# Kernel tuning notes

Hardware: AMD Instinct MI355X
Metric: run time of the kernel (lower is better)

Reference implementation:

```python
import jax, jax.numpy as jnp
import numpy as np

B, T, D = 4, 2048, 1024
H = 16
HD = D // H  # 64


def setup_inputs() -> dict:
    key = jax.random.key(0)
    k1, k2, k3 = jax.random.split(key, 3)
    x = jax.random.normal(k1, (B, T, D), dtype=jnp.float32)
    w_qkv = jax.random.normal(k2, (D, 3 * D), dtype=jnp.float32) * (1.0 / np.sqrt(D))
    w_out = jax.random.normal(k3, (D, D), dtype=jnp.float32) * (1.0 / np.sqrt(D))
    return {"x": x, "w_qkv": w_qkv, "w_out": w_out}


def reference(x, w_qkv, w_out):
    b, t, c = x.shape
    qkv = x @ w_qkv  # [B,T,3D]
    q, k, v = jnp.split(qkv, 3, axis=-1)

    def heads(u):
        return u.reshape(b, t, H, HD).transpose(0, 2, 1, 3)  # [B,H,T,HD]

    q, k, v = heads(q), heads(k), heads(v)
    scale = 1.0 / np.sqrt(HD).astype(np.float32)
    attn = jnp.einsum('bhqd,bhkd->bhqk', q, k) * scale  # [B,H,T,T]
    causal = jnp.tril(jnp.ones((t, t), dtype=bool))
    attn = jnp.where(causal[None, None, :, :], attn, -jnp.inf)
    attn = jax.nn.softmax(attn, axis=-1)
    y = jnp.einsum('bhqk,bhkd->bhqd', attn, v)  # [B,H,T,HD]
    y = y.transpose(0, 2, 1, 3).reshape(b, t, c)
    return y @ w_out
```

## Files before the change

kernel.cpp:

```cpp
#include <hip/hip_runtime.h>
#include <hip/hip_bf16.h>
#include <stdint.h>

#define B_    4
#define T_    2048
#define D_    1024
#define H_    16
#define HD_   64
#define ROWS_ (B_ * T_)
#define NQKV_ (3 * D_)

typedef __attribute__((ext_vector_type(8))) short bf16x8;
typedef __attribute__((ext_vector_type(4))) float f32x4;

__device__ __forceinline__ unsigned short f2bf(float f) {
    union { float f; uint32_t u; } v; v.f = f;
    uint32_t u = v.u;
    return (unsigned short)((u + 0x7FFFu + ((u >> 16) & 1u)) >> 16);
}

__device__ __forceinline__ void glds16(const unsigned short* g, unsigned short* l) {
    __builtin_amdgcn_global_load_lds(
        (const __attribute__((address_space(1))) void*)g,
        (__attribute__((address_space(3))) void*)l, 16, 0, 0);
}

__global__ void cvt_bf16_kernel(const float* __restrict__ in,
                                unsigned short* __restrict__ out, int n8) {
    int i = blockIdx.x * blockDim.x + threadIdx.x;
    if (i >= n8) return;
    float4 a = ((const float4*)in)[2 * i];
    float4 b = ((const float4*)in)[2 * i + 1];
    union { bf16x8 v; unsigned short s[8]; } o;
    o.s[0] = f2bf(a.x); o.s[1] = f2bf(a.y); o.s[2] = f2bf(a.z); o.s[3] = f2bf(a.w);
    o.s[4] = f2bf(b.x); o.s[5] = f2bf(b.y); o.s[6] = f2bf(b.z); o.s[7] = f2bf(b.w);
    ((bf16x8*)out)[i] = o.v;
}

__global__ __launch_bounds__(256) void tcvt_kernel(const float* __restrict__ in,
                                                   unsigned short* __restrict__ out,
                                                   int K, int N, int ncut, float scale) {
    __shared__ float tile[64 * 65];
    const int t = threadIdx.x;
    const int n0 = blockIdx.x * 64, k0 = blockIdx.y * 64;
#pragma unroll
    for (int it = 0; it < 4; ++it) {
        int id = it * 256 + t;
        int r = id >> 4, c = (id & 15) * 4;
        float4 v = *(const float4*)&in[(size_t)(k0 + r) * N + n0 + c];
        tile[r * 65 + c + 0] = v.x; tile[r * 65 + c + 1] = v.y;
        tile[r * 65 + c + 2] = v.z; tile[r * 65 + c + 3] = v.w;
    }
    __syncthreads();
#pragma unroll
    for (int it = 0; it < 2; ++it) {
        int id = it * 256 + t;
        int n = id >> 3, kc = (id & 7) * 8;
        float sc = (n0 + n < ncut) ? scale : 1.0f;
        union { bf16x8 v; unsigned short s[8]; } o;
#pragma unroll
        for (int i = 0; i < 8; ++i) o.s[i] = f2bf(tile[(kc + i) * 65 + n] * sc);
        *(bf16x8*)&out[(size_t)(n0 + n) * K + k0 + kc] = o.v;
    }
}

template<int OUT_BF16, int VSPLIT>
__global__ __launch_bounds__(256) void gemm128_kernel(
    const unsigned short* __restrict__ A,
    const unsigned short* __restrict__ Bt,
    void* __restrict__ Cp, int M, int K, int ldC,
    unsigned short* __restrict__ vt)
{
    __shared__ __align__(16) unsigned short As[128 * 32];
    __shared__ __align__(16) unsigned short Bs[128 * 32];

    const int t = threadIdx.x, w = t >> 6, lane = t & 63;
    const int wm = w >> 1, wn = w & 1;
    const int lm = lane & 15, lq = lane >> 4;
    const int m0 = blockIdx.y * 128, n0 = blockIdx.x * 128;

    f32x4 acc[4][4];
#pragma unroll
    for (int i = 0; i < 4; i++)
#pragma unroll
        for (int j = 0; j < 4; j++) acc[i][j] = (f32x4){0.f, 0.f, 0.f, 0.f};

    const int id0 = t, id1 = 256 + t;
    const unsigned short* Ap0 = A + (size_t)(m0 + (id0 >> 2)) * K + (id0 & 3) * 8;
    const unsigned short* Ap1 = A + (size_t)(m0 + (id1 >> 2)) * K + (id1 & 3) * 8;
    const unsigned short* Bp0 = Bt + (size_t)(n0 + (id0 >> 2)) * K + (id0 & 3) * 8;
    const unsigned short* Bp1 = Bt + (size_t)(n0 + (id1 >> 2)) * K + (id1 & 3) * 8;

    for (int k0 = 0; k0 < K; k0 += 32) {
        __syncthreads();
        glds16(Ap0 + k0, &As[id0 * 8]);
        glds16(Ap1 + k0, &As[id1 * 8]);
        glds16(Bp0 + k0, &Bs[id0 * 8]);
        glds16(Bp1 + k0, &Bs[id1 * 8]);
        __syncthreads();

        bf16x8 af[4], bfr[4];
#pragma unroll
        for (int mt = 0; mt < 4; mt++)
            af[mt] = *(const bf16x8*)&As[(wm * 64 + mt * 16 + lm) * 32 + lq * 8];
#pragma unroll
        for (int nt = 0; nt < 4; nt++)
            bfr[nt] = *(const bf16x8*)&Bs[(wn * 64 + nt * 16 + lm) * 32 + lq * 8];
#pragma unroll
        for (int mt = 0; mt < 4; mt++)
#pragma unroll
            for (int nt = 0; nt < 4; nt++)
                acc[mt][nt] = __builtin_amdgcn_mfma_f32_16x16x32_bf16(
                    af[mt], bfr[nt], acc[mt][nt], 0, 0, 0);
    }

    if (VSPLIT && n0 >= 2048) {
#pragma unroll
        for (int mt = 0; mt < 4; mt++)
#pragma unroll
            for (int nt = 0; nt < 4; nt++)
#pragma unroll
                for (int r = 0; r < 4; r++) {
                    int row = m0 + wm * 64 + mt * 16 + lq * 4 + r;
                    int col = n0 + wn * 64 + nt * 16 + lm - 2048;
                    int bb = row >> 11, tt = row & 2047;
                    size_t vi = ((size_t)((bb * 16 + (col >> 6)) * 64 + (col & 63))) * 2048 + tt;
                    vt[vi] = f2bf(acc[mt][nt][r]);
                }
        return;
    }
#pragma unroll
    for (int mt = 0; mt < 4; mt++)
#pragma unroll
        for (int nt = 0; nt < 4; nt++)
#pragma unroll
            for (int r = 0; r < 4; r++) {
                int row = m0 + wm * 64 + mt * 16 + lq * 4 + r;
                int col = n0 + wn * 64 + nt * 16 + lm;
                if (OUT_BF16)
                    ((unsigned short*)Cp)[(size_t)row * ldC + col] = f2bf(acc[mt][nt][r]);
                else
                    ((float*)Cp)[(size_t)row * ldC + col] = acc[mt][nt][r];
            }
}

__global__ __launch_bounds__(256) void attn3_kernel(
    const unsigned short* __restrict__ qk,
    const unsigned short* __restrict__ vt,
    unsigned short* __restrict__ y)
{
    __shared__ __align__(16) unsigned short Ks[64 * 72];
    __shared__ __align__(16) unsigned short Vs[64 * 72];
    __shared__ __align__(16) unsigned short Ps[4][32 * 72];

    const int bh = blockIdx.x, pair = blockIdx.y;
    const int b = bh >> 4, h = bh & 15;
    const int t = threadIdx.x, w = t >> 6, lane = t & 63;
    const int lm = lane & 15, lq = lane >> 4;
    unsigned short* psw = Ps[w];

    const bf16x8 onesf = {0x3F80, 0x3F80, 0x3F80, 0x3F80,
                          0x3F80, 0x3F80, 0x3F80, 0x3F80};

    for (int which = 0; which < 2; ++which) {
        const int qt = which ? pair : (15 - pair);
        const int q0 = qt * 128, qw0 = q0 + w * 32;

        bf16x8 qf[2][2];
#pragma unroll
        for (int mt = 0; mt < 2; mt++)
#pragma unroll
            for (int kk = 0; kk < 2; kk++)
                qf[mt][kk] = *(const bf16x8*)
                    &qk[(size_t)(b * T_ + qw0 + mt * 16 + lm) * 2048 + h * HD_ + kk * 32 + lq * 8];

        f32x4 o[2][4], osum[2];
#pragma unroll
        for (int mt = 0; mt < 2; mt++) {
            osum[mt] = (f32x4){0.f, 0.f, 0.f, 0.f};
#pragma unroll
            for (int dt = 0; dt < 4; dt++) o[mt][dt] = (f32x4){0.f, 0.f, 0.f, 0.f};
        }

        const int kend = q0 + 128;
        for (int kt = 0; kt < kend; kt += 64) {
            __syncthreads();
#pragma unroll
            for (int it = 0; it < 2; ++it) {
                int id = it * 256 + t;
                int rr = id >> 3, cc = (id & 7) * 8;
                *(bf16x8*)&Ks[rr * 72 + cc] = *(const bf16x8*)
                    &qk[(size_t)(b * T_ + kt + rr) * 2048 + D_ + h * HD_ + cc];
                *(bf16x8*)&Vs[rr * 72 + cc] = *(const bf16x8*)
                    &vt[(size_t)(bh * 64 + rr) * 2048 + kt + cc];
            }
            __syncthreads();
            if (kt >= qw0 + 32) continue;

            f32x4 s[2][4];
#pragma unroll
            for (int mt = 0; mt < 2; mt++)
#pragma unroll
                for (int nt = 0; nt < 4; nt++) s[mt][nt] = (f32x4){0.f, 0.f, 0.f, 0.f};
#pragma unroll
            for (int nt = 0; nt < 4; nt++)
#pragma unroll
                for (int kk = 0; kk < 2; kk++) {
                    bf16x8 kf = *(const bf16x8*)&Ks[(nt * 16 + lm) * 72 + kk * 32 + lq * 8];
#pragma unroll
                    for (int mt = 0; mt < 2; mt++)
                        s[mt][nt] = __builtin_amdgcn_mfma_f32_16x16x32_bf16(
                            qf[mt][kk], kf, s[mt][nt], 0, 0, 0);
                }

            const bool need_mask = (kt + 64 > qw0);
            if (need_mask) {
#pragma unroll
                for (int mt = 0; mt < 2; mt++)
#pragma unroll
                    for (int nt = 0; nt < 4; nt++)
#pragma unroll
                        for (int r = 0; r < 4; r++) {
                            int qi = qw0 + mt * 16 + lq * 4 + r;
                            int kj = kt + nt * 16 + lm;
                            float p = (kj <= qi) ? exp2f(s[mt][nt][r]) : 0.f;
                            psw[(mt * 16 + lq * 4 + r) * 72 + nt * 16 + lm] = f2bf(p);
                        }
            } else {
#pragma unroll
                for (int mt = 0; mt < 2; mt++)
#pragma unroll
                    for (int nt = 0; nt < 4; nt++)
#pragma unroll
                        for (int r = 0; r < 4; r++)
                            psw[(mt * 16 + lq * 4 + r) * 72 + nt * 16 + lm]
                                = f2bf(exp2f(s[mt][nt][r]));
            }

#pragma unroll
            for (int kk = 0; kk < 2; kk++) {
                bf16x8 pf0 = *(const bf16x8*)&psw[(lm) * 72 + kk * 32 + lq * 8];
                bf16x8 pf1 = *(const bf16x8*)&psw[(16 + lm) * 72 + kk * 32 + lq * 8];
                osum[0] = __builtin_amdgcn_mfma_f32_16x16x32_bf16(pf0, onesf, osum[0], 0, 0, 0);
                osum[1] = __builtin_amdgcn_mfma_f32_16x16x32_bf16(pf1, onesf, osum[1], 0, 0, 0);
#pragma unroll
                for (int dt = 0; dt < 4; dt++) {
                    bf16x8 vf = *(const bf16x8*)&Vs[(dt * 16 + lm) * 72 + kk * 32 + lq * 8];
                    o[0][dt] = __builtin_amdgcn_mfma_f32_16x16x32_bf16(pf0, vf, o[0][dt], 0, 0, 0);
                    o[1][dt] = __builtin_amdgcn_mfma_f32_16x16x32_bf16(pf1, vf, o[1][dt], 0, 0, 0);
                }
            }
        }

#pragma unroll
        for (int mt = 0; mt < 2; mt++)
#pragma unroll
            for (int r = 0; r < 4; r++) {
                float rli = 1.f / osum[mt][r];
#pragma unroll
                for (int dt = 0; dt < 4; dt++)
                    y[(size_t)(b * T_ + qw0 + mt * 16 + lq * 4 + r) * D_ + h * HD_ + dt * 16 + lm]
                        = f2bf(o[mt][dt][r] * rli);
            }
    }
}

extern "C" void kernel_launch(void* const* d_in, const int* in_sizes, int n_in,
                              void* d_out, int out_size, void* d_ws, size_t ws_size,
                              hipStream_t stream) {
    const float* x    = (const float*)d_in[0];
    const float* wqkv = (const float*)d_in[1];
    const float* wout = (const float*)d_in[2];
    float* out = (float*)d_out;

    char* ws = (char*)d_ws;
    unsigned short* xb     = (unsigned short*)ws; ws += (size_t)ROWS_ * D_ * 2;
    unsigned short* wqkvbt = (unsigned short*)ws; ws += (size_t)D_ * NQKV_ * 2;
    unsigned short* woutbt = (unsigned short*)ws; ws += (size_t)D_ * D_ * 2;
    unsigned short* qkb    = (unsigned short*)ws; ws += (size_t)ROWS_ * 2048 * 2;
    unsigned short* vtb    = (unsigned short*)ws; ws += (size_t)ROWS_ * D_ * 2;
    unsigned short* yb     = (unsigned short*)ws;

    const float SC = 0.18033688011112042f;

    cvt_bf16_kernel<<<ROWS_ * D_ / 8 / 256, 256, 0, stream>>>(x, xb, ROWS_ * D_ / 8);
    tcvt_kernel<<<dim3(NQKV_ / 64, D_ / 64), 256, 0, stream>>>(wqkv, wqkvbt, D_, NQKV_, D_, SC);
    tcvt_kernel<<<dim3(D_ / 64, D_ / 64), 256, 0, stream>>>(wout, woutbt, D_, D_, 0, 1.0f);

    gemm128_kernel<1, 1><<<dim3(NQKV_ / 128, ROWS_ / 128), 256, 0, stream>>>(
        xb, wqkvbt, qkb, ROWS_, D_, 2048, vtb);

    attn3_kernel<<<dim3(B_ * H_, 8), 256, 0, stream>>>(qkb, vtb, yb);

    gemm128_kernel<0, 0><<<dim3(D_ / 128, ROWS_ / 128), 256, 0, stream>>>(
        yb, woutbt, out, ROWS_, D_, D_, nullptr);
}
```

Before: 274.6 us.

## Prefetch K/V tiles into registers, transpose QK^T MFMA, vectorize P and V stores

The attention kernel now issues the global loads for the next K/V tile into registers before computing on the current one, so load latency overlaps compute. QK^T is computed transposed (K as the A operand), which lets each lane hold 4 consecutive keys and write P to LDS as packed 8-byte stores using truncation rounding and the hardware exp2 intrinsic. The V-transpose epilogue of the QKV GEMM also packs four bf16 values into one 8-byte store. This adds register pressure and truncates P instead of rounding to nearest.

```diff
diff --git a/kernel.cpp b/kernel.cpp
--- a/kernel.cpp
+++ b/kernel.cpp
@@ -17,6 +17,11 @@
     union { float f; uint32_t u; } v; v.f = f;
     uint32_t u = v.u;
     return (unsigned short)((u + 0x7FFFu + ((u >> 16) & 1u)) >> 16);
+}
+
+__device__ __forceinline__ uint32_t pack2_rtz(float a, float b) {
+    union { float f; uint32_t u; } x, y; x.f = a; y.f = b;
+    return (x.u >> 16) | (y.u & 0xFFFF0000u);
 }
 
 __device__ __forceinline__ void glds16(const unsigned short* g, unsigned short* l) {
@@ -118,15 +123,16 @@
 #pragma unroll
         for (int mt = 0; mt < 4; mt++)
 #pragma unroll
-            for (int nt = 0; nt < 4; nt++)
-#pragma unroll
-                for (int r = 0; r < 4; r++) {
-                    int row = m0 + wm * 64 + mt * 16 + lq * 4 + r;
-                    int col = n0 + wn * 64 + nt * 16 + lm - 2048;
-                    int bb = row >> 11, tt = row & 2047;
-                    size_t vi = ((size_t)((bb * 16 + (col >> 6)) * 64 + (col & 63))) * 2048 + tt;
-                    vt[vi] = f2bf(acc[mt][nt][r]);
-                }
+            for (int nt = 0; nt < 4; nt++) {
+                int row0 = m0 + wm * 64 + mt * 16 + lq * 4;
+                int col  = n0 + wn * 64 + nt * 16 + lm - 2048;
+                int bb = row0 >> 11, tt = row0 & 2047;
+                size_t vi = ((size_t)((bb * 16 + (col >> 6)) * 64 + (col & 63))) * 2048 + tt;
+                uint2 pk;
+                pk.x = (uint32_t)f2bf(acc[mt][nt][0]) | ((uint32_t)f2bf(acc[mt][nt][1]) << 16);
+                pk.y = (uint32_t)f2bf(acc[mt][nt][2]) | ((uint32_t)f2bf(acc[mt][nt][3]) << 16);
+                *(uint2*)&vt[vi] = pk;
+            }
         return;
     }
 #pragma unroll
@@ -144,7 +150,7 @@
             }
 }
 
-__global__ __launch_bounds__(256) void attn3_kernel(
+__global__ __launch_bounds__(256) void attn4_kernel(
     const unsigned short* __restrict__ qk,
     const unsigned short* __restrict__ vt,
     unsigned short* __restrict__ y)
@@ -159,6 +165,11 @@
     const int lm = lane & 15, lq = lane >> 4;
     unsigned short* psw = Ps[w];
 
+    const int r0 = t >> 3,           c0 = (t & 7) * 8;
+    const int r1 = (256 + t) >> 3,   c1 = (t & 7) * 8;
+    const unsigned short* kgb = qk + (size_t)(b * T_) * 2048 + D_ + h * HD_;
+    const unsigned short* vgb = vt + (size_t)(bh * 64) * 2048;
+
     const bf16x8 onesf = {0x3F80, 0x3F80, 0x3F80, 0x3F80,
                           0x3F80, 0x3F80, 0x3F80, 0x3F80};
 
@@ -183,25 +194,31 @@
         }
 
         const int kend = q0 + 128;
+
+        bf16x8 ka = *(const bf16x8*)&kgb[(size_t)(0 + r0) * 2048 + c0];
+        bf16x8 kb = *(const bf16x8*)&kgb[(size_t)(0 + r1) * 2048 + c1];
+        bf16x8 va = *(const bf16x8*)&vgb[(size_t)r0 * 2048 + 0 + c0];
+        bf16x8 vb = *(const bf16x8*)&vgb[(size_t)r1 * 2048 + 0 + c1];
+
         for (int kt = 0; kt < kend; kt += 64) {
             __syncthreads();
-#pragma unroll
-            for (int it = 0; it < 2; ++it) {
-                int id = it * 256 + t;
-                int rr = id >> 3, cc = (id & 7) * 8;
-                *(bf16x8*)&Ks[rr * 72 + cc] = *(const bf16x8*)
-                    &qk[(size_t)(b * T_ + kt + rr) * 2048 + D_ + h * HD_ + cc];
-                *(bf16x8*)&Vs[rr * 72 + cc] = *(const bf16x8*)
-                    &vt[(size_t)(bh * 64 + rr) * 2048 + kt + cc];
-            }
+            *(bf16x8*)&Ks[r0 * 72 + c0] = ka;
+            *(bf16x8*)&Ks[r1 * 72 + c1] = kb;
+            *(bf16x8*)&Vs[r0 * 72 + c0] = va;
+            *(bf16x8*)&Vs[r1 * 72 + c1] = vb;
+            int ktn = (kt + 64 < kend) ? kt + 64 : kt;
+            ka = *(const bf16x8*)&kgb[(size_t)(ktn + r0) * 2048 + c0];
+            kb = *(const bf16x8*)&kgb[(size_t)(ktn + r1) * 2048 + c1];
+            va = *(const bf16x8*)&vgb[(size_t)r0 * 2048 + ktn + c0];
+            vb = *(const bf16x8*)&vgb[(size_t)r1 * 2048 + ktn + c1];
             __syncthreads();
             if (kt >= qw0 + 32) continue;
 
-            f32x4 s[2][4];
-#pragma unroll
-            for (int mt = 0; mt < 2; mt++)
-#pragma unroll
-                for (int nt = 0; nt < 4; nt++) s[mt][nt] = (f32x4){0.f, 0.f, 0.f, 0.f};
+            f32x4 st[4][2];
+#pragma unroll
+            for (int nt = 0; nt < 4; nt++)
+#pragma unroll
+                for (int mt = 0; mt < 2; mt++) st[nt][mt] = (f32x4){0.f, 0.f, 0.f, 0.f};
 #pragma unroll
             for (int nt = 0; nt < 4; nt++)
 #pragma unroll
@@ -209,32 +226,33 @@
                     bf16x8 kf = *(const bf16x8*)&Ks[(nt * 16 + lm) * 72 + kk * 32 + lq * 8];
 #pragma unroll
                     for (int mt = 0; mt < 2; mt++)
-                        s[mt][nt] = __builtin_amdgcn_mfma_f32_16x16x32_bf16(
-                            qf[mt][kk], kf, s[mt][nt], 0, 0, 0);
+                        st[nt][mt] = __builtin_amdgcn_mfma_f32_16x16x32_bf16(
+                            kf, qf[mt][kk], st[nt][mt], 0, 0, 0);
                 }
 
-            const bool need_mask = (kt + 64 > qw0);
-            if (need_mask) {
-#pragma unroll
-                for (int mt = 0; mt < 2; mt++)
-#pragma unroll
-                    for (int nt = 0; nt < 4; nt++)
-#pragma unroll
-                        for (int r = 0; r < 4; r++) {
-                            int qi = qw0 + mt * 16 + lq * 4 + r;
-                            int kj = kt + nt * 16 + lm;
-                            float p = (kj <= qi) ? exp2f(s[mt][nt][r]) : 0.f;
-                            psw[(mt * 16 + lq * 4 + r) * 72 + nt * 16 + lm] = f2bf(p);
-                        }
-            } else {
-#pragma unroll
-                for (int mt = 0; mt < 2; mt++)
-#pragma unroll
-                    for (int nt = 0; nt < 4; nt++)
+            const bool diag = (kt + 64 > qw0);
+#pragma unroll
+            for (int mt = 0; mt < 2; mt++) {
+                const int qi = qw0 + mt * 16 + lm;
+#pragma unroll
+                for (int nt = 0; nt < 4; nt++) {
+                    float p[4];
+                    if (diag) {
+                        const int kj0 = kt + nt * 16 + lq * 4;
 #pragma unroll
                         for (int r = 0; r < 4; r++)
-                            psw[(mt * 16 + lq * 4 + r) * 72 + nt * 16 + lm]
-                                = f2bf(exp2f(s[mt][nt][r]));
+                            p[r] = (kj0 + r <= qi)
+                                 ? __builtin_amdgcn_exp2f(st[nt][mt][r]) : 0.f;
+                    } else {
+#pragma unroll
+                        for (int r = 0; r < 4; r++)
+                            p[r] = __builtin_amdgcn_exp2f(st[nt][mt][r]);
+                    }
+                    uint2 pk;
+                    pk.x = pack2_rtz(p[0], p[1]);
+                    pk.y = pack2_rtz(p[2], p[3]);
+                    *(uint2*)&psw[(mt * 16 + lm) * 72 + nt * 16 + lq * 4] = pk;
+                }
             }
 
 #pragma unroll
@@ -290,7 +308,7 @@
     gemm128_kernel<1, 1><<<dim3(NQKV_ / 128, ROWS_ / 128), 256, 0, stream>>>(
         xb, wqkvbt, qkb, ROWS_, D_, 2048, vtb);
 
-    attn3_kernel<<<dim3(B_ * H_, 8), 256, 0, stream>>>(qkb, vtb, yb);
+    attn4_kernel<<<dim3(B_ * H_, 8), 256, 0, stream>>>(qkb, vtb, yb);
 
     gemm128_kernel<0, 0><<<dim3(D_ / 128, ROWS_ / 128), 256, 0, stream>>>(
         yb, woutbt, out, ROWS_, D_, D_, nullptr);
```

New measurement: 260.6 us. 1.05x faster.
